# Optimization experiments

Measured on AMD Instinct MI355X. Metric: run time of the kernel, lower is better.

The kernel has to match this reference:

```python
import jax, jax.numpy as jnp
import numpy as np

B, K, H, W, N = 256, 16, 64, 64, 1024   # batch, channels (n_ch), grid H/W, sampled sites
F_IN = 9 * K - 1                         # 3x3 neighborhood * K channels, minus center channel


def setup_inputs() -> dict:
    key = jax.random.key(0)
    ks = jax.random.split(key, 8)
    z_int = jax.random.randint(ks[0], (B, K, H, W), 0, 16, dtype=jnp.int32)
    bs = jax.random.randint(ks[1], (N,), 0, K, dtype=jnp.int32)
    ii = jax.random.randint(ks[2], (N,), 0, H, dtype=jnp.int32)
    jj = jax.random.randint(ks[3], (N,), 0, W, dtype=jnp.int32)
    W1 = jax.random.normal(ks[4], (F_IN, 128), dtype=jnp.float32) * 0.05
    b1 = jnp.zeros((128,), dtype=jnp.float32)
    W2 = jax.random.normal(ks[5], (128, 16), dtype=jnp.float32) * 0.05
    b2 = jnp.zeros((16,), dtype=jnp.float32)
    return {"z_int": z_int, "bs": bs, "ii": ii, "jj": jj,
            "W1": W1, "b1": b1, "W2": W2, "b2": b2}


def _gather_ctx(z_f, bs, ii, jj):
    # Faithful to get_context ordering: loops di, dj (each in [-1,0,1]) then b,
    # skipping (di==0, dj==0, b==bi). Flattened skip position = 4*K + bi.
    off = jnp.array([-1, 0, 1], dtype=jnp.int32)
    di = jnp.repeat(off, 3)          # [9]
    dj = jnp.tile(off, 3)            # [9]
    ni = (ii[:, None] + di[None, :]) % H   # [N, 9] toroidal wrap
    nj = (jj[:, None] + dj[None, :]) % W   # [N, 9]
    ctx = z_f[:, :, ni, nj]                # [B, K, N, 9]
    ctx = jnp.transpose(ctx, (2, 0, 3, 1)).reshape(N, B, 9 * K)  # [N, B, 9K], (di,dj) major then b
    drop = 4 * K + bs                      # [N] center-channel flat index
    idx = jnp.arange(F_IN, dtype=jnp.int32)
    keep = idx[None, :] + (idx[None, :] >= drop[:, None]).astype(jnp.int32)  # [N, F_IN]
    return jax.vmap(lambda c, k: c[:, k])(ctx, keep)  # [N, B, F_IN]


def reference(z_int, bs, ii, jj, W1, b1, W2, b2):
    z_f = z_int.astype(jnp.float32) / 15.0
    ctx = _gather_ctx(z_f, bs, ii, jj)                 # [N, B, 9K-1]
    h = jax.nn.relu(jnp.einsum('nbf,fh->nbh', ctx, W1) + b1)
    logits = jnp.einsum('nbh,hc->nbc', h, W2) + b2     # [N, B, 16]
    pred = jnp.argmax(logits, axis=-1)                 # [N, B]
    tgt = z_int[:, bs, ii, jj].T                       # [N, B]
    rate = jnp.mean((pred != tgt).astype(jnp.float32)) # np.mean of per-site mean == global mean
    return rate
```

## Files before the change

kernel.cpp:

```cpp
#include <hip/hip_runtime.h>
#include <stdint.h>

#define NB 1024
#define BB 256
#define KK 16
#define HH 64
#define WW 64
#define F_FULL 144
#define HDIM 128
#define CDIM 16
#define KPAD 160
#define APITCH 168
#define HPITCH 136
#define ABYTES (64 * APITCH * 2)

typedef __bf16 bf16x8 __attribute__((ext_vector_type(8)));
typedef float f32x4 __attribute__((ext_vector_type(4)));

#define W1T_OFF 256
#define W1T_BYTES (16 * HDIM * KPAD * 2)
#define W2B_OFF (W1T_OFF + W1T_BYTES)
#define W2B_BYTES (CDIM * HDIM * 2)
#define ZT_OFF (W2B_OFF + W2B_BYTES)

__device__ __forceinline__ unsigned short bf16_bits(float v) {
    __bf16 b = (__bf16)v;
    return __builtin_bit_cast(unsigned short, b);
}

#define TP 144
__global__ __launch_bounds__(256) void prep_kernel(
    const int* __restrict__ z, const float* __restrict__ W1,
    const float* __restrict__ W2, uint8_t* __restrict__ zt,
    unsigned short* __restrict__ W1t, unsigned short* __restrict__ W2b,
    int* __restrict__ counters) {
    int bid = blockIdx.x;
    int t = threadIdx.x;
    if (bid < 4096) {
        __shared__ uint8_t tile[32 * TP];
        int bx = bid & 127;
        int by = bid >> 7;
        int c0 = bx * 32, r0 = by * 128;
#pragma unroll
        for (int i = 0; i < 4; ++i) {
            int lin = i * 256 + t;
            int c = lin & 31;
            int rq = lin >> 5;
            uchar4 v;
            v.x = (uint8_t)z[(size_t)(r0 + rq * 4 + 0) * 4096 + c0 + c];
            v.y = (uint8_t)z[(size_t)(r0 + rq * 4 + 1) * 4096 + c0 + c];
            v.z = (uint8_t)z[(size_t)(r0 + rq * 4 + 2) * 4096 + c0 + c];
            v.w = (uint8_t)z[(size_t)(r0 + rq * 4 + 3) * 4096 + c0 + c];
            *(uchar4*)(tile + c * TP + rq * 4) = v;
        }
        __syncthreads();
        int cy = t >> 3, rx = t & 7;
        uint4 v = *(const uint4*)(tile + cy * TP + rx * 16);
        *(uint4*)(zt + (size_t)(c0 + cy) * 4096 + r0 + rx * 16) = v;
    } else if (bid < 5376) {
        int idx = (bid - 4096) * 256 + t;
        int k = idx % KPAD;
        int h = (idx / KPAD) % HDIM;
        int s = idx / (KPAD * HDIM);
        int drop = 4 * KK + s;
        float val = 0.0f;
        if (k < F_FULL && k != drop) {
            int src = k - (k > drop ? 1 : 0);
            val = W1[src * HDIM + h];
        }
        W1t[idx] = bf16_bits(val);
    } else {
        int idx = (bid - 5376) * 256 + t;
        if (idx < CDIM * HDIM) {
            int k = idx % HDIM;
            int c = idx / HDIM;
            W2b[idx] = bf16_bits(W2[k * CDIM + c]);
        }
        if (bid == 5376 && t == 0) counters[0] = 0;
    }
}

__global__ __launch_bounds__(256, 3) void main_kernel(
    const uint8_t* __restrict__ zt, const unsigned short* __restrict__ W1t,
    const float* __restrict__ b1, const unsigned short* __restrict__ W2b,
    const float* __restrict__ b2, const int* __restrict__ bs,
    const int* __restrict__ ii, const int* __restrict__ jj,
    int* __restrict__ counters) {
    __shared__ __align__(16) unsigned char smem[2 * ABYTES + 64 * 17 * 4];
    unsigned short* sA0 = (unsigned short*)smem;
    unsigned short* sA1 = (unsigned short*)(smem + ABYTES);
    float* slg = (float*)(smem + 2 * ABYTES);

    int t = threadIdx.x;
    int n = blockIdx.x;
    int wave = t >> 6, lane = t & 63;
    int l15 = lane & 15, l4 = lane >> 4;

    int in_ = ii[n], jn = jj[n], sn = bs[n];

    const unsigned short* w1s = W1t + (size_t)sn * (HDIM * KPAD);
    int n0 = wave * 32;
    bf16x8 Bf[2][5];
#pragma unroll
    for (int nt = 0; nt < 2; ++nt)
#pragma unroll
        for (int ks = 0; ks < 5; ++ks)
            Bf[nt][ks] = *(const bf16x8*)(w1s + (n0 + nt * 16 + l15) * KPAD + ks * 32 + l4 * 8);
    bf16x8 Bf2[4];
#pragma unroll
    for (int ks = 0; ks < 4; ++ks)
        Bf2[ks] = *(const bf16x8*)(W2b + l15 * HDIM + ks * 32 + l4 * 8);
    float b1v0 = b1[n0 + l15], b1v1 = b1[n0 + 16 + l15];
    float b2v = b2[l15];

    if (t < 192) {
        int b = t / 3, part = t % 3;
        *(uint4*)(sA0 + b * APITCH + F_FULL + part * 8) = make_uint4(0, 0, 0, 0);
        *(uint4*)(sA1 + b * APITCH + F_FULL + part * 8) = make_uint4(0, 0, 0, 0);
    }

    uint4 g0, g1, g2;
    auto gload = [&](int tile) {
        int b = (t & 63) + tile * 64;
        int p0 = t >> 6;
        int ni0 = (in_ + p0 / 3 - 1) & (HH - 1);
        int nj0 = (jn + p0 % 3 - 1) & (WW - 1);
        g0 = *(const uint4*)(zt + (((size_t)(ni0 * WW + nj0) * BB + b) << 4));
        int p1 = p0 + 4;
        int ni1 = (in_ + p1 / 3 - 1) & (HH - 1);
        int nj1 = (jn + p1 % 3 - 1) & (WW - 1);
        g1 = *(const uint4*)(zt + (((size_t)(ni1 * WW + nj1) * BB + b) << 4));
        if (t < 64) {
            int ni2 = (in_ + 1) & (HH - 1);
            int nj2 = (jn + 1) & (WW - 1);
            g2 = *(const uint4*)(zt + (((size_t)(ni2 * WW + nj2) * BB + b) << 4));
        }
    };
    auto gwrite = [&](unsigned short* dst) {
        int b = t & 63;
        int p0 = t >> 6;
        auto conv = [&](uint4 raw, int p) {
            const uint8_t* bytes = (const uint8_t*)&raw;
            union { __bf16 h[16]; uint4 q[2]; } u;
#pragma unroll
            for (int k = 0; k < 16; ++k)
                u.h[k] = (__bf16)((float)bytes[k] * (1.0f / 15.0f));
            uint4* d = (uint4*)(dst + b * APITCH + p * 16);
            d[0] = u.q[0];
            d[1] = u.q[1];
        };
        conv(g0, p0);
        conv(g1, p0 + 4);
        if (t < 64) conv(g2, 8);
    };

    gload(0);
    gwrite(sA0);
    int local_err = 0;

    for (int tile = 0; tile < 4; ++tile) {
        unsigned short* sA = (tile & 1) ? sA1 : sA0;
        unsigned short* sH = sA;
        unsigned short* sAnext = (tile & 1) ? sA0 : sA1;

        if (tile < 3) gload(tile + 1);
        __syncthreads();

        f32x4 acc[4][2] = {};
#pragma unroll
        for (int mt = 0; mt < 4; ++mt) {
            bf16x8 Af[5];
#pragma unroll
            for (int ks = 0; ks < 5; ++ks)
                Af[ks] = *(const bf16x8*)(sA + (mt * 16 + l15) * APITCH + ks * 32 + l4 * 8);
#pragma unroll
            for (int ks = 0; ks < 5; ++ks) {
                acc[mt][0] = __builtin_amdgcn_mfma_f32_16x16x32_bf16(Af[ks], Bf[0][ks], acc[mt][0], 0, 0, 0);
                acc[mt][1] = __builtin_amdgcn_mfma_f32_16x16x32_bf16(Af[ks], Bf[1][ks], acc[mt][1], 0, 0, 0);
            }
        }
        __syncthreads();

#pragma unroll
        for (int mt = 0; mt < 4; ++mt)
#pragma unroll
            for (int nt = 0; nt < 2; ++nt) {
                float bv = nt ? b1v1 : b1v0;
                int hcol = n0 + nt * 16 + l15;
#pragma unroll
                for (int r = 0; r < 4; ++r) {
                    int b = mt * 16 + l4 * 4 + r;
                    float v = fmaxf(acc[mt][nt][r] + bv, 0.0f);
                    sH[b * HPITCH + hcol] = bf16_bits(v);
                }
            }
        __syncthreads();

        f32x4 acc2 = {};
#pragma unroll
        for (int ks = 0; ks < 4; ++ks) {
            bf16x8 Af = *(const bf16x8*)(sH + (wave * 16 + l15) * HPITCH + ks * 32 + l4 * 8);
            acc2 = __builtin_amdgcn_mfma_f32_16x16x32_bf16(Af, Bf2[ks], acc2, 0, 0, 0);
        }
#pragma unroll
        for (int r = 0; r < 4; ++r) {
            int b = wave * 16 + l4 * 4 + r;
            slg[b * 17 + l15] = acc2[r] + b2v;
        }
        __syncthreads();

        if (t < 64) {
            float best = slg[t * 17];
            int pi = 0;
#pragma unroll
            for (int c = 1; c < CDIM; ++c) {
                float v = slg[t * 17 + c];
                if (v > best) { best = v; pi = c; }
            }
            int bglob = tile * 64 + t;
            int tgt = zt[(((size_t)(in_ * WW + jn) * BB + bglob) << 4) + sn];
            unsigned long long m = __ballot(pi != tgt);
            if (t == 0) local_err += (int)__popcll(m);
        }
        if (tile < 3) gwrite(sAnext);
    }

    if (t == 0) atomicAdd(&counters[0], local_err);
}

__global__ void finalize_kernel(const int* __restrict__ counters, float* __restrict__ out) {
    out[0] = (float)(counters[0]) / (float)(NB * BB);
}

extern "C" void kernel_launch(void* const* d_in, const int* in_sizes, int n_in,
                              void* d_out, int out_size, void* d_ws, size_t ws_size,
                              hipStream_t stream) {
    const int* z = (const int*)d_in[0];
    const int* bs = (const int*)d_in[1];
    const int* ii = (const int*)d_in[2];
    const int* jj = (const int*)d_in[3];
    const float* W1 = (const float*)d_in[4];
    const float* b1 = (const float*)d_in[5];
    const float* W2 = (const float*)d_in[6];
    const float* b2 = (const float*)d_in[7];
    float* out = (float*)d_out;

    uint8_t* ws = (uint8_t*)d_ws;
    int* counters = (int*)ws;
    unsigned short* W1t = (unsigned short*)(ws + W1T_OFF);
    unsigned short* W2b = (unsigned short*)(ws + W2B_OFF);
    uint8_t* zt = ws + ZT_OFF;

    prep_kernel<<<5384, 256, 0, stream>>>(z, W1, W2, zt, W1t, W2b, counters);
    main_kernel<<<NB, 256, 0, stream>>>(zt, W1t, b1, W2b, b2, bs, ii, jj, counters);
    finalize_kernel<<<1, 1, 0, stream>>>(counters, out);
}
```

Measured before the change: 135.3 us.

## Split sites across batch-tile blocks, vectorize transpose loads, shuffle argmax, spread counters

Main kernel now launches one block per (site, 64-batch tile) instead of looping over four tiles per block. It drops the double-buffered shared memory and raises occupancy to 4 blocks per CU, with block ids remapped so neighbouring blocks share a site. The prep transpose reads z with 16-byte vector loads and packs four bytes per word. Argmax now uses wave shuffles instead of a shared-memory logits pass, and errors go to 128 counters that a 64-thread finalize reduces. The trade is that W1 fragments are reloaded four times as often, and the tile-to-tile load overlap is given up.

```diff
diff --git a/kernel.cpp b/kernel.cpp
--- a/kernel.cpp
+++ b/kernel.cpp
@@ -13,11 +13,12 @@
 #define APITCH 168
 #define HPITCH 136
 #define ABYTES (64 * APITCH * 2)
+#define NCTR 128
 
 typedef __bf16 bf16x8 __attribute__((ext_vector_type(8)));
 typedef float f32x4 __attribute__((ext_vector_type(4)));
 
-#define W1T_OFF 256
+#define W1T_OFF 1024
 #define W1T_BYTES (16 * HDIM * KPAD * 2)
 #define W2B_OFF (W1T_OFF + W1T_BYTES)
 #define W2B_BYTES (CDIM * HDIM * 2)
@@ -41,18 +42,18 @@
         int bx = bid & 127;
         int by = bid >> 7;
         int c0 = bx * 32, r0 = by * 128;
-#pragma unroll
-        for (int i = 0; i < 4; ++i) {
-            int lin = i * 256 + t;
-            int c = lin & 31;
-            int rq = lin >> 5;
-            uchar4 v;
-            v.x = (uint8_t)z[(size_t)(r0 + rq * 4 + 0) * 4096 + c0 + c];
-            v.y = (uint8_t)z[(size_t)(r0 + rq * 4 + 1) * 4096 + c0 + c];
-            v.z = (uint8_t)z[(size_t)(r0 + rq * 4 + 2) * 4096 + c0 + c];
-            v.w = (uint8_t)z[(size_t)(r0 + rq * 4 + 3) * 4096 + c0 + c];
-            *(uchar4*)(tile + c * TP + rq * 4) = v;
-        }
+        int rq4 = t >> 3;
+        int cq = t & 7;
+        const int* zp = z + (size_t)(r0 + rq4 * 4) * 4096 + c0 + cq * 4;
+        uint4 v0 = *(const uint4*)(zp);
+        uint4 v1 = *(const uint4*)(zp + 4096);
+        uint4 v2 = *(const uint4*)(zp + 8192);
+        uint4 v3 = *(const uint4*)(zp + 12288);
+        uint32_t* tw = (uint32_t*)tile;
+        tw[(cq * 4 + 0) * 36 + rq4] = v0.x | (v1.x << 8) | (v2.x << 16) | (v3.x << 24);
+        tw[(cq * 4 + 1) * 36 + rq4] = v0.y | (v1.y << 8) | (v2.y << 16) | (v3.y << 24);
+        tw[(cq * 4 + 2) * 36 + rq4] = v0.z | (v1.z << 8) | (v2.z << 16) | (v3.z << 24);
+        tw[(cq * 4 + 3) * 36 + rq4] = v0.w | (v1.w << 8) | (v2.w << 16) | (v3.w << 24);
         __syncthreads();
         int cy = t >> 3, rx = t & 7;
         uint4 v = *(const uint4*)(tile + cy * TP + rx * 16);
@@ -76,27 +77,46 @@
             int c = idx / HDIM;
             W2b[idx] = bf16_bits(W2[k * CDIM + c]);
         }
-        if (bid == 5376 && t == 0) counters[0] = 0;
-    }
-}
-
-__global__ __launch_bounds__(256, 3) void main_kernel(
+        if (bid == 5376 && t < NCTR) counters[t] = 0;
+    }
+}
+
+__global__ __launch_bounds__(256, 4) void main_kernel(
     const uint8_t* __restrict__ zt, const unsigned short* __restrict__ W1t,
     const float* __restrict__ b1, const unsigned short* __restrict__ W2b,
     const float* __restrict__ b2, const int* __restrict__ bs,
     const int* __restrict__ ii, const int* __restrict__ jj,
     int* __restrict__ counters) {
-    __shared__ __align__(16) unsigned char smem[2 * ABYTES + 64 * 17 * 4];
-    unsigned short* sA0 = (unsigned short*)smem;
-    unsigned short* sA1 = (unsigned short*)(smem + ABYTES);
-    float* slg = (float*)(smem + 2 * ABYTES);
+    __shared__ __align__(16) unsigned char smem[ABYTES];
+    unsigned short* sA = (unsigned short*)smem;
+    unsigned short* sH = sA;
 
     int t = threadIdx.x;
-    int n = blockIdx.x;
+    int bid = blockIdx.x;
+    int n = (bid & 7) | ((bid >> 5) << 3);
+    int bt = (bid >> 3) & 3;
     int wave = t >> 6, lane = t & 63;
     int l15 = lane & 15, l4 = lane >> 4;
 
     int in_ = ii[n], jn = jj[n], sn = bs[n];
+
+    int b64 = (t & 63) + bt * 64;
+    uint4 g0, g1, g2;
+    {
+        int p0 = t >> 6;
+        int ni0 = (in_ + p0 / 3 - 1) & (HH - 1);
+        int nj0 = (jn + p0 % 3 - 1) & (WW - 1);
+        g0 = *(const uint4*)(zt + (((size_t)(ni0 * WW + nj0) * BB + b64) << 4));
+        int p1 = p0 + 4;
+        int ni1 = (in_ + p1 / 3 - 1) & (HH - 1);
+        int nj1 = (jn + p1 % 3 - 1) & (WW - 1);
+        g1 = *(const uint4*)(zt + (((size_t)(ni1 * WW + nj1) * BB + b64) << 4));
+        if (t < 64) {
+            int ni2 = (in_ + 1) & (HH - 1);
+            int nj2 = (jn + 1) & (WW - 1);
+            g2 = *(const uint4*)(zt + (((size_t)(ni2 * WW + nj2) * BB + b64) << 4));
+        }
+    }
 
     const unsigned short* w1s = W1t + (size_t)sn * (HDIM * KPAD);
     int n0 = wave * 32;
@@ -106,38 +126,16 @@
 #pragma unroll
         for (int ks = 0; ks < 5; ++ks)
             Bf[nt][ks] = *(const bf16x8*)(w1s + (n0 + nt * 16 + l15) * KPAD + ks * 32 + l4 * 8);
-    bf16x8 Bf2[4];
-#pragma unroll
-    for (int ks = 0; ks < 4; ++ks)
-        Bf2[ks] = *(const bf16x8*)(W2b + l15 * HDIM + ks * 32 + l4 * 8);
     float b1v0 = b1[n0 + l15], b1v1 = b1[n0 + 16 + l15];
     float b2v = b2[l15];
 
     if (t < 192) {
-        int b = t / 3, part = t % 3;
-        *(uint4*)(sA0 + b * APITCH + F_FULL + part * 8) = make_uint4(0, 0, 0, 0);
-        *(uint4*)(sA1 + b * APITCH + F_FULL + part * 8) = make_uint4(0, 0, 0, 0);
-    }
-
-    uint4 g0, g1, g2;
-    auto gload = [&](int tile) {
-        int b = (t & 63) + tile * 64;
-        int p0 = t >> 6;
-        int ni0 = (in_ + p0 / 3 - 1) & (HH - 1);
-        int nj0 = (jn + p0 % 3 - 1) & (WW - 1);
-        g0 = *(const uint4*)(zt + (((size_t)(ni0 * WW + nj0) * BB + b) << 4));
-        int p1 = p0 + 4;
-        int ni1 = (in_ + p1 / 3 - 1) & (HH - 1);
-        int nj1 = (jn + p1 % 3 - 1) & (WW - 1);
-        g1 = *(const uint4*)(zt + (((size_t)(ni1 * WW + nj1) * BB + b) << 4));
-        if (t < 64) {
-            int ni2 = (in_ + 1) & (HH - 1);
-            int nj2 = (jn + 1) & (WW - 1);
-            g2 = *(const uint4*)(zt + (((size_t)(ni2 * WW + nj2) * BB + b) << 4));
-        }
-    };
-    auto gwrite = [&](unsigned short* dst) {
-        int b = t & 63;
+        int bb = t / 3, part = t % 3;
+        *(uint4*)(sA + bb * APITCH + F_FULL + part * 8) = make_uint4(0, 0, 0, 0);
+    }
+
+    {
+        int bloc = t & 63;
         int p0 = t >> 6;
         auto conv = [&](uint4 raw, int p) {
             const uint8_t* bytes = (const uint8_t*)&raw;
@@ -145,91 +143,83 @@
 #pragma unroll
             for (int k = 0; k < 16; ++k)
                 u.h[k] = (__bf16)((float)bytes[k] * (1.0f / 15.0f));
-            uint4* d = (uint4*)(dst + b * APITCH + p * 16);
+            uint4* d = (uint4*)(sA + bloc * APITCH + p * 16);
             d[0] = u.q[0];
             d[1] = u.q[1];
         };
         conv(g0, p0);
         conv(g1, p0 + 4);
         if (t < 64) conv(g2, 8);
-    };
-
-    gload(0);
-    gwrite(sA0);
-    int local_err = 0;
-
-    for (int tile = 0; tile < 4; ++tile) {
-        unsigned short* sA = (tile & 1) ? sA1 : sA0;
-        unsigned short* sH = sA;
-        unsigned short* sAnext = (tile & 1) ? sA0 : sA1;
-
-        if (tile < 3) gload(tile + 1);
-        __syncthreads();
-
-        f32x4 acc[4][2] = {};
-#pragma unroll
-        for (int mt = 0; mt < 4; ++mt) {
-            bf16x8 Af[5];
-#pragma unroll
-            for (int ks = 0; ks < 5; ++ks)
-                Af[ks] = *(const bf16x8*)(sA + (mt * 16 + l15) * APITCH + ks * 32 + l4 * 8);
-#pragma unroll
-            for (int ks = 0; ks < 5; ++ks) {
-                acc[mt][0] = __builtin_amdgcn_mfma_f32_16x16x32_bf16(Af[ks], Bf[0][ks], acc[mt][0], 0, 0, 0);
-                acc[mt][1] = __builtin_amdgcn_mfma_f32_16x16x32_bf16(Af[ks], Bf[1][ks], acc[mt][1], 0, 0, 0);
+    }
+    __syncthreads();
+
+    f32x4 acc[4][2] = {};
+#pragma unroll
+    for (int mt = 0; mt < 4; ++mt) {
+        bf16x8 Af[5];
+#pragma unroll
+        for (int ks = 0; ks < 5; ++ks)
+            Af[ks] = *(const bf16x8*)(sA + (mt * 16 + l15) * APITCH + ks * 32 + l4 * 8);
+#pragma unroll
+        for (int ks = 0; ks < 5; ++ks) {
+            acc[mt][0] = __builtin_amdgcn_mfma_f32_16x16x32_bf16(Af[ks], Bf[0][ks], acc[mt][0], 0, 0, 0);
+            acc[mt][1] = __builtin_amdgcn_mfma_f32_16x16x32_bf16(Af[ks], Bf[1][ks], acc[mt][1], 0, 0, 0);
+        }
+    }
+    __syncthreads();
+
+#pragma unroll
+    for (int mt = 0; mt < 4; ++mt)
+#pragma unroll
+        for (int nt = 0; nt < 2; ++nt) {
+            float bv = nt ? b1v1 : b1v0;
+            int hcol = n0 + nt * 16 + l15;
+#pragma unroll
+            for (int r = 0; r < 4; ++r) {
+                int b = mt * 16 + l4 * 4 + r;
+                float v = fmaxf(acc[mt][nt][r] + bv, 0.0f);
+                sH[b * HPITCH + hcol] = bf16_bits(v);
             }
         }
-        __syncthreads();
-
-#pragma unroll
-        for (int mt = 0; mt < 4; ++mt)
-#pragma unroll
-            for (int nt = 0; nt < 2; ++nt) {
-                float bv = nt ? b1v1 : b1v0;
-                int hcol = n0 + nt * 16 + l15;
-#pragma unroll
-                for (int r = 0; r < 4; ++r) {
-                    int b = mt * 16 + l4 * 4 + r;
-                    float v = fmaxf(acc[mt][nt][r] + bv, 0.0f);
-                    sH[b * HPITCH + hcol] = bf16_bits(v);
-                }
-            }
-        __syncthreads();
-
-        f32x4 acc2 = {};
-#pragma unroll
-        for (int ks = 0; ks < 4; ++ks) {
-            bf16x8 Af = *(const bf16x8*)(sH + (wave * 16 + l15) * HPITCH + ks * 32 + l4 * 8);
-            acc2 = __builtin_amdgcn_mfma_f32_16x16x32_bf16(Af, Bf2[ks], acc2, 0, 0, 0);
-        }
-#pragma unroll
-        for (int r = 0; r < 4; ++r) {
-            int b = wave * 16 + l4 * 4 + r;
-            slg[b * 17 + l15] = acc2[r] + b2v;
-        }
-        __syncthreads();
-
-        if (t < 64) {
-            float best = slg[t * 17];
-            int pi = 0;
-#pragma unroll
-            for (int c = 1; c < CDIM; ++c) {
-                float v = slg[t * 17 + c];
-                if (v > best) { best = v; pi = c; }
-            }
-            int bglob = tile * 64 + t;
-            int tgt = zt[(((size_t)(in_ * WW + jn) * BB + bglob) << 4) + sn];
-            unsigned long long m = __ballot(pi != tgt);
-            if (t == 0) local_err += (int)__popcll(m);
-        }
-        if (tile < 3) gwrite(sAnext);
-    }
-
-    if (t == 0) atomicAdd(&counters[0], local_err);
+    __syncthreads();
+
+    bf16x8 Bf2[4];
+#pragma unroll
+    for (int ks = 0; ks < 4; ++ks)
+        Bf2[ks] = *(const bf16x8*)(W2b + l15 * HDIM + ks * 32 + l4 * 8);
+    f32x4 acc2 = {};
+#pragma unroll
+    for (int ks = 0; ks < 4; ++ks) {
+        bf16x8 Af = *(const bf16x8*)(sH + (wave * 16 + l15) * HPITCH + ks * 32 + l4 * 8);
+        acc2 = __builtin_amdgcn_mfma_f32_16x16x32_bf16(Af, Bf2[ks], acc2, 0, 0, 0);
+    }
+
+    int err = 0;
+    size_t tbase = ((size_t)(in_ * WW + jn) * BB) << 4;
+#pragma unroll
+    for (int r = 0; r < 4; ++r) {
+        float v = acc2[r] + b2v;
+        int idx = l15;
+#pragma unroll
+        for (int m = 1; m < 16; m <<= 1) {
+            float ov = __shfl_xor(v, m);
+            int oi = __shfl_xor(idx, m);
+            if (ov > v || (ov == v && oi < idx)) { v = ov; idx = oi; }
+        }
+        int bg = bt * 64 + wave * 16 + l4 * 4 + r;
+        int tgt = zt[tbase + ((size_t)bg << 4) + sn];
+        unsigned long long mm = __ballot(l15 == 0 && idx != tgt);
+        err += (int)__popcll(mm);
+    }
+    if (lane == 0) atomicAdd(&counters[bid & (NCTR - 1)], err);
 }
 
 __global__ void finalize_kernel(const int* __restrict__ counters, float* __restrict__ out) {
-    out[0] = (float)(counters[0]) / (float)(NB * BB);
+    int t = threadIdx.x;
+    int s = counters[t] + counters[t + 64];
+#pragma unroll
+    for (int m = 32; m; m >>= 1) s += __shfl_down(s, m);
+    if (t == 0) out[0] = (float)s / (float)(NB * BB);
 }
 
 extern "C" void kernel_launch(void* const* d_in, const int* in_sizes, int n_in,
@@ -252,6 +242,6 @@
     uint8_t* zt = ws + ZT_OFF;
 
     prep_kernel<<<5384, 256, 0, stream>>>(z, W1, W2, zt, W1t, W2b, counters);
-    main_kernel<<<NB, 256, 0, stream>>>(zt, W1t, b1, W2b, b2, bs, ii, jj, counters);
-    finalize_kernel<<<1, 1, 0, stream>>>(counters, out);
-}
+    main_kernel<<<NB * 4, 256, 0, stream>>>(zt, W1t, b1, W2b, b2, bs, ii, jj, counters);
+    finalize_kernel<<<1, 64, 0, stream>>>(counters, out);
+}
```

Result: slower. 153.6 us (+13.5%).
